# Kernel optimization log

Measured on AMD Instinct MI355X. Metric: run time of the kernel, lower is better.

The kernel has to match this reference:

```python
import jax, jax.numpy as jnp
import numpy as np
from jax.scipy.special import erfinv

N, F0, F1 = 256, 128, 64          # nodes, scalar channels, vector channels
RB, KSEQ, EMB = 32, 16, 32        # radial bins, seq window, pos-embed dim
RC = 24.0                         # radial_cut
NI = F0 + F1                      # num output irreps (per-irrep scalar gate)
CIN = F0 + F1 + 1 + F0            # 321 = per-l fan-in of the message Linear

# real l=2 CG matrices, e3nn component order: (xz, xy, y^2-(x^2+z^2)/2, yz, z^2-x^2)
_M = np.zeros((5, 3, 3), np.float32)
_M[0, 0, 2] = _M[0, 2, 0] = 1.0 / np.sqrt(10.0)
_M[1, 0, 1] = _M[1, 1, 0] = 1.0 / np.sqrt(10.0)
_M[2] = np.diag([-1.0, 2.0, -1.0]) / np.sqrt(30.0)
_M[3, 1, 2] = _M[3, 2, 1] = 1.0 / np.sqrt(10.0)
_M[4] = np.diag([-1.0, 0.0, 1.0]) / np.sqrt(10.0)
M2 = jnp.asarray(_M)

# e3nn-style normalized activation: silu / sqrt(E[silu(z)^2]), z ~ N(0,1)
_zs = jnp.sqrt(2.0) * erfinv(jnp.linspace(-1.0 + 1e-6, 1.0 - 1e-6, 100001))
C_SILU = jnp.sqrt(jnp.mean(jax.nn.silu(_zs) ** 2))

def nsilu(x):
    return jax.nn.silu(x) / C_SILU

def setup_inputs() -> dict:
    key = jax.random.key(0)
    ks = jax.random.split(key, 12)
    return {
        "feat": jax.random.normal(ks[0], (N, F0 + 3 * F1), jnp.float32),
        "coord": 8.0 * jax.random.normal(ks[1], (N, 3), jnp.float32),
        "W_msg0": jax.random.normal(ks[2], (CIN, F0), jnp.float32),
        "W_msg1": jax.random.normal(ks[3], (CIN, F1), jnp.float32),
        "embed_tbl": jax.random.normal(ks[4], (2 * KSEQ + 1, EMB), jnp.float32) / jnp.sqrt(2.0 * KSEQ + 1.0),
        "W_mlp1": jax.random.normal(ks[5], (EMB + RB + F0 + F0, RB), jnp.float32),
        "W_mlp2": jax.random.normal(ks[6], (RB, NI), jnp.float32),
        "W_out0": jax.random.normal(ks[7], (F0, F0), jnp.float32),
        "W_out1": jax.random.normal(ks[8], (F1, F1), jnp.float32),
        "W_move": jax.random.normal(ks[9], (F1, 1), jnp.float32),
        "mask": jax.random.randint(ks[10], (N,), 0, 2).astype(bool),
    }

def reference(feat, coord, W_msg0, W_msg1, embed_tbl, W_mlp1, W_mlp2, W_out0, W_out1, W_move, mask):
    n = feat.shape[0]
    s_in = feat[:, :F0]                       # [N,128] scalar irreps
    v_in = feat[:, F0:].reshape(n, F1, 3)     # [N,64,3] vector irreps
    cm = mask[:, None] & mask[None, :]
    cmf = cm.astype(feat.dtype)
    vec = (coord[:, None, :] - coord[None, :, :]) * cmf[..., None]   # [N,N,3]
    nsq = jnp.sum(vec ** 2, -1)
    dist = jnp.sqrt(jnp.where(nsq == 0.0, 1.0, nsq))
    x, y, z = vec[..., 0], vec[..., 1], vec[..., 2]
    # spherical harmonics, normalize=False, component normalization
    sh1 = jnp.sqrt(3.0) * vec
    sh2 = jnp.stack([jnp.sqrt(15.0) * x * z, jnp.sqrt(15.0) * x * y,
                     jnp.sqrt(5.0) * (y * y - 0.5 * (x * x + z * z)),
                     jnp.sqrt(15.0) * y * z, jnp.sqrt(15.0) / 2.0 * (z * z - x * x)], -1)
    # ---- message Linear over concat([TP(ang, feat_j), ang, feat_j]) ----
    # 0e inputs: [N,N,321]
    in0 = jnp.concatenate([
        cmf[..., None] * s_in[None, :, :],                        # 0e(sh) x 0e
        jnp.einsum('abd,bcd->abc', sh1, v_in) / jnp.sqrt(3.0),    # 1o x 1o -> 0e
        cmf[..., None],                                           # ang 0e (masked)
        jnp.broadcast_to(s_in[None], (n, n, F0)),                 # feat_j 0e
    ], -1)
    msg0 = jnp.einsum('abi,io->abo', in0, W_msg0) / jnp.sqrt(float(CIN))   # [N,N,128]
    # 1o inputs: [N,N,321,3]
    in1 = jnp.concatenate([
        cmf[..., None, None] * v_in[None],                                 # 0e x 1o
        sh1[:, :, None, :] * s_in[None, :, :, None],                       # 1o x 0e
        jnp.sqrt(3.0) * jnp.einsum('abm,mdk,bcd->abck', sh2, M2, v_in),    # 2e x 1o -> 1o
        sh1[:, :, None, :],                                                # ang 1o
        jnp.broadcast_to(v_in[None], (n, n, F1, 3)),                       # feat_j 1o
    ], 2)
    msg1 = jnp.einsum('abid,io->abod', in1, W_msg1) / jnp.sqrt(float(CIN))  # [N,N,64,3]
    # ---- radial / sequence gate ----
    values = jnp.linspace(0.0, RC, RB + 2)[1:-1]
    step = values[1] - values[0]
    rad = jnp.exp(-(((dist[..., None] - values) / step) ** 2)) / 1.12 * cmf[..., None]
    pos = jnp.arange(n)
    rel = pos[:, None] - pos[None, :]
    rel = jnp.where(jnp.abs(rel) <= KSEQ, rel, 0)
    rel = jnp.where(cm, rel, 0) + KSEQ
    pemb = embed_tbl[rel]                                                  # [N,N,32]
    gate_in = jnp.concatenate([pemb, rad,
                               jnp.broadcast_to(s_in[:, None, :], (n, n, F0)),
                               msg0], -1)                                  # [N,N,320]
    h = nsilu(jnp.einsum('abi,io->abo', gate_in, W_mlp1) / jnp.sqrt(float(gate_in.shape[-1])))
    gate = jnp.einsum('abi,io->abo', h, W_mlp2) / jnp.sqrt(float(RB))      # [N,N,192]
    msg0 = msg0 * gate[..., :F0] * cmf[..., None]
    msg1 = msg1 * gate[..., F0:, None] * cmf[..., None, None]
    # ---- masked mean aggregation over j ----
    cnt = jnp.sum(cmf, 1, keepdims=True)
    aggr0 = jnp.sum(msg0, 1) / (cnt + 1e-6)
    aggr1 = jnp.sum(msg1, 1) / (cnt[..., None] + 1e-6)
    keep = (cnt > 1).astype(feat.dtype)
    aggr0 = aggr0 * keep
    aggr1 = aggr1 * keep[..., None]
    # output Linear per irrep type
    f0 = aggr0 @ W_out0 / jnp.sqrt(float(F0))
    f1 = jnp.einsum('ncd,co->nod', aggr1, W_out1) / jnp.sqrt(float(F1))
    # coordinate update (move=True)
    coord_new = coord + 0.001 * jnp.einsum('ncd,co->nod', f1, W_move)[:, 0, :] / jnp.sqrt(float(F1))
    # residual + equivariant layer norm
    r0 = s_in + f0
    r1 = v_in + f1
    mu = jnp.mean(r0, -1, keepdims=True)
    n0 = (r0 - mu) / jnp.sqrt(jnp.var(r0, -1, keepdims=True) + 1e-6)
    rms = jnp.sqrt(jnp.mean(r1 ** 2, (-2, -1), keepdims=True) + 1e-6)
    n1 = r1 / rms
    return jnp.concatenate([n0, n1.reshape(n, -1), coord_new], -1)   # [N, 323]
```

## Files before the change

### kernel.cpp

```cpp
#include <hip/hip_runtime.h>
#include <math.h>

#define NN 256
#define NSPLIT 2

#define OFF_T0    0
#define OFF_TW    131072
#define OFF_T1A   163840
#define OFF_T1B   229376
#define OFF_S     294912
#define OFF_E     303104
#define OFF_CSP   305152
#define OFF_PART  305472
#define OFF_NA    469312
#define OFF_MASKD 469376

__device__ __forceinline__ float my_erfinv(float x){
    float w = -logf((1.0f - x) * (1.0f + x));
    float p;
    if (w < 5.0f) {
        w = w - 2.5f;
        p = 2.81022636e-08f;
        p = 3.43273939e-07f + p*w;
        p = -3.5233877e-06f + p*w;
        p = -4.39150654e-06f + p*w;
        p = 0.00021858087f  + p*w;
        p = -0.00125372503f + p*w;
        p = -0.00417768164f + p*w;
        p = 0.246640727f    + p*w;
        p = 1.50140941f     + p*w;
    } else {
        w = sqrtf(w) - 3.0f;
        p = -0.000200214257f;
        p = 0.000100950558f + p*w;
        p = 0.00134934322f  + p*w;
        p = -0.00367342844f + p*w;
        p = 0.00573950773f  + p*w;
        p = -0.0076224613f  + p*w;
        p = 0.00943887047f  + p*w;
        p = 1.00167406f     + p*w;
        p = 2.83297682f     + p*w;
    }
    return p * x;
}

__global__ __launch_bounds__(256) void precompute_kernel(
    const float* __restrict__ feat, const float* __restrict__ W0,
    const float* __restrict__ W1, const float* __restrict__ tbl,
    const float* __restrict__ Wm1, float* __restrict__ ws)
{
    int b = blockIdx.x, t = threadIdx.x;
    __shared__ float s_l[128], v_l[192];
    __shared__ float P0B_l[128], V0_l[3][128];
    __shared__ float red[256];

    if (b >= NN){
        int bi = b - NN;
        int lo = bi * 391;
        int hi = lo + 391; if (hi > 100001) hi = 100001;
        float acc = 0.f;
        for (int i = lo + t; i < hi; i += 256){
            float u = -0.999999f + (float)i * (1.999998f / 100000.0f);
            float z = 1.41421356237f * my_erfinv(u);
            float s = z / (1.0f + __expf(-z));
            acc += s * s;
        }
        red[t] = acc;
        __syncthreads();
        for (int off = 128; off >= 1; off >>= 1){
            if (t < off) red[t] += red[t + off];
            __syncthreads();
        }
        if (t == 0) ws[OFF_CSP + bi] = red[0];
        return;
    }

    for (int idx = t; idx < 320; idx += 256){
        float val = feat[b*320 + idx];
        if (idx < 128) s_l[idx] = val; else v_l[idx-128] = val;
    }
    __syncthreads();
    if (t < 128){
        int o = t;
        float p0 = W0[192*128 + o];
        #pragma unroll 4
        for (int i = 0; i < 128; i++){
            float s = s_l[i];
            p0 += s * (W0[i*128 + o] + W0[(193+i)*128 + o]);
        }
        float v0d[3];
        for (int d = 0; d < 3; d++){
            float v0 = 0.f;
            #pragma unroll 4
            for (int c = 0; c < 64; c++) v0 += v_l[c*3+d] * W0[(128+c)*128 + o];
            v0d[d] = v0;
        }
        P0B_l[o] = p0;
        V0_l[0][o] = v0d[0]; V0_l[1][o] = v0d[1]; V0_l[2][o] = v0d[2];
        ((float4*)(ws + OFF_T0))[b*128 + o] = make_float4(p0, v0d[0], v0d[1], v0d[2]);
    } else if (t < 192){
        int o = t - 128;
        float ac[3];
        for (int k = 0; k < 3; k++){
            float s = 0.f;
            #pragma unroll 4
            for (int c = 0; c < 64; c++){
                float v = v_l[c*3+k];
                s += v * (W1[c*64 + o] + W1[(257+c)*64 + o]);
            }
            ac[k] = s;
        }
        float p1 = W1[256*64 + o];
        #pragma unroll 4
        for (int c = 0; c < 128; c++) p1 += s_l[c] * W1[(64+c)*64 + o];
        float u1[3];
        for (int d = 0; d < 3; d++){
            float s = 0.f;
            #pragma unroll 4
            for (int c = 0; c < 64; c++) s += v_l[c*3+d] * W1[(192+c)*64 + o];
            u1[d] = 1.73205081f * s;
        }
        ((float4*)(ws + OFF_T1A))[b*64 + o] = make_float4(ac[0], ac[1], ac[2], p1);
        ((float4*)(ws + OFF_T1B))[b*64 + o] = make_float4(u1[0], u1[1], u1[2], 0.f);
    } else if (t < 224){
        int r = t - 192;
        float s = 0.f;
        #pragma unroll 4
        for (int i = 0; i < 128; i++) s += s_l[i] * Wm1[(64+i)*32 + r];
        ws[OFF_S + b*32 + r] = s;
        if (b < 33){
            float e = 0.f;
            #pragma unroll 4
            for (int k = 0; k < 32; k++) e += tbl[b*32 + k] * Wm1[k*32 + r];
            ws[OFF_E + b*32 + r] = e;
        }
    }
    __syncthreads();
    if (t < 32){
        int r = t;
        float pw = 0.f, vw0 = 0.f, vw1 = 0.f, vw2 = 0.f;
        #pragma unroll 4
        for (int o = 0; o < 128; o++){
            float w = Wm1[(192+o)*32 + r];
            pw  += P0B_l[o]  * w;
            vw0 += V0_l[0][o]* w;
            vw1 += V0_l[1][o]* w;
            vw2 += V0_l[2][o]* w;
        }
        ((float4*)(ws + OFF_TW))[b*32 + r] = make_float4(pw, vw0, vw1, vw2);
    }
}

__global__ __launch_bounds__(512) void main_kernel(
    const float* __restrict__ coord, const int* __restrict__ maskraw,
    const float* __restrict__ Wm1, const float* __restrict__ Wm2,
    float* __restrict__ ws, float* __restrict__ part)
{
    const int bid = blockIdx.x;
    const int a = bid >> 1;
    const int q = bid & 1;
    const int t = threadIdx.x;
    const int g = t >> 5;
    const int l = t & 31;

    __shared__ __align__(16) float smem_big[192*36];
    __shared__ __align__(16) float WT1[32*36];
    __shared__ __align__(16) float E_l[33*32];
    __shared__ __align__(16) float hsh[16*32];
    __shared__ __align__(16) float radsh[16*32];
    __shared__ int   blist[NN];
    __shared__ float cxl[NN], cyl[NN], czl[NN];
    __shared__ int   wcnt[4], wbase[4];
    __shared__ float cs_part[4];
    __shared__ int   na_sh, bflag_sh, maska_sh;
    __shared__ float invc_sh;

    for (int idx = t; idx < 6144; idx += 512){
        int r = idx / 192, o = idx - r*192;
        smem_big[o*36 + r] = Wm2[idx];
    }
    for (int idx = t; idx < 1024; idx += 512){
        int j = idx >> 5, l2 = idx & 31;
        WT1[l2*36 + j] = Wm1[1024 + idx];
    }
    for (int idx = t; idx < 1056; idx += 512) E_l[idx] = ws[OFF_E + idx];

    if (t == 0) bflag_sh = 0;
    __syncthreads();
    if (t < 64 && (maskraw[t] & 0xFFFFFFFE)) bflag_sh = 1;
    float cs_acc = (t < NN) ? ws[OFF_CSP + t] : 0.f;
    __syncthreads();
    const bool bytemode = bflag_sh != 0;

    int m_t = 0, pfx = 0;
    if (t < NN){
        if (bytemode){
            unsigned int w = (unsigned int)maskraw[t >> 2];
            m_t = ((w >> ((t & 3) * 8)) & 0xFFu) != 0;
        } else {
            m_t = maskraw[t] != 0;
        }
        if (t == a) maska_sh = m_t;
        if (bid == 0) ((int*)ws)[OFF_MASKD + t] = m_t;
        unsigned long long bal = __ballot(m_t != 0);
        int lane = t & 63;
        pfx = __popcll(bal & ((1ull << lane) - 1ull));
        if (lane == 0) wcnt[t >> 6] = __popcll(bal);
        #pragma unroll
        for (int off = 32; off >= 1; off >>= 1) cs_acc += __shfl_xor(cs_acc, off);
        if (lane == 0) cs_part[t >> 6] = cs_acc;
    }
    __syncthreads();
    if (t == 0){
        int s = 0;
        for (int w = 0; w < 4; w++){ wbase[w] = s; s += wcnt[w]; }
        na_sh = s;
        if (bid == 0) ((int*)ws)[OFF_NA] = s;
        float cstot = cs_part[0] + cs_part[1] + cs_part[2] + cs_part[3];
        invc_sh = 1.0f / sqrtf(cstot / 100001.0f);
    }
    __syncthreads();
    if (t < NN && m_t) blist[wbase[t >> 6] + pfx] = t;
    __syncthreads();
    const int na_all = na_sh;
    for (int idx = t; idx < na_all; idx += 512){
        int bb = blist[idx];
        cxl[idx] = coord[bb*3+0];
        cyl[idx] = coord[bb*3+1];
        czl[idx] = coord[bb*3+2];
    }
    __syncthreads();

    const float inv_c = invc_sh;
    const bool mask_a = maska_sh != 0;
    const float ca0 = coord[a*3+0], ca1 = coord[a*3+1], ca2 = coord[a*3+2];
    const float sar = ws[OFF_S + a*32 + l];

    const float ISC   = 0.055814557f;
    const float IS320 = 0.055901699f;

    float acc0[4] = {0.f,0.f,0.f,0.f};
    float acc1[2][3] = {{0.f,0.f,0.f},{0.f,0.f,0.f}};

    const int na_eff = mask_a ? na_all : 0;
    const int nq = (na_eff + NSPLIT - 1) / NSPLIT;
    const int base = q * nq;
    int cntq = na_eff - base;
    if (cntq < 0) cntq = 0;
    if (cntq > nq) cntq = nq;
    const int iters = (cntq + 15) >> 4;

    const float4* T0  = (const float4*)(ws + OFF_T0);
    const float4* TW  = (const float4*)(ws + OFF_TW);
    const float4* T1A = (const float4*)(ws + OFF_T1A);
    const float4* T1B = (const float4*)(ws + OFF_T1B);
    const float4* Wm2T4 = (const float4*)smem_big;
    const float4* WT14  = (const float4*)WT1;

    for (int i = 0; i < iters; i++){
        int il = i*16 + g;
        bool active = il < cntq;
        int idx = base + (active ? il : 0);
        int b = blist[idx];
        float cmf = active ? 1.0f : 0.0f;

        float vx = ca0 - cxl[idx], vy = ca1 - cyl[idx], vz = ca2 - czl[idx];
        float nsq = vx*vx + vy*vy + vz*vz;
        float dist = sqrtf(nsq == 0.0f ? 1.0f : nsq);
        float sh1x = 1.73205081f*vx, sh1y = 1.73205081f*vy, sh1z = 1.73205081f*vz;
        float s20 = 3.87298335f*vx*vz;
        float s21 = 3.87298335f*vx*vy;
        float s22 = 2.23606798f*(vy*vy - 0.5f*(vx*vx + vz*vz));
        float s23 = 3.87298335f*vy*vz;
        float s24 = 1.93649167f*(vz*vz - vx*vx);
        float Txx = -s22*0.182574186f - s24*0.316227766f;
        float Tyy =  s22*0.365148372f;
        float Tzz = -s22*0.182574186f + s24*0.316227766f;
        float Txy =  s21*0.316227766f;
        float Txz =  s20*0.316227766f;
        float Tyz =  s23*0.316227766f;

        float m0v[4];
        #pragma unroll
        for (int j = 0; j < 4; j++){
            float4 t0 = T0[b*128 + l + 32*j];
            m0v[j] = t0.x + vx*t0.y + vy*t0.z + vz*t0.w;
        }

        float vcen = 0.727272727f * (float)(l + 1);
        float ddr = (dist - vcen) * 1.375f;
        float rl = __expf(-ddr*ddr) * 0.892857143f * cmf;
        radsh[g*32 + l] = rl;
        float radw = 0.f;
        {
            const float4* rv = (const float4*)radsh + g*8;
            const float4* wv = WT14 + l*9;
            #pragma unroll
            for (int j4 = 0; j4 < 8; j4++){
                float4 r4 = rv[j4];
                float4 w4 = wv[j4];
                radw += r4.x*w4.x + r4.y*w4.y + r4.z*w4.z + r4.w*w4.w;
            }
        }

        int ir = a - b;
        if (ir > 16 || ir < -16) ir = 0;
        if (!active) ir = 0;
        ir += 16;
        float4 tw = TW[b*32 + l];
        float msgblk = tw.x + vx*tw.y + vy*tw.z + vz*tw.w;
        float pre = (E_l[ir*32 + l] + sar + radw + msgblk*ISC) * IS320;
        float h = pre / (1.0f + __expf(-pre)) * inv_c;
        hsh[g*32 + l] = h;

        float gg[6] = {0,0,0,0,0,0};
        {
            const float4* hv = (const float4*)hsh + g*8;
            #pragma unroll
            for (int r4 = 0; r4 < 8; r4++){
                float4 h4 = hv[r4];
                #pragma unroll
                for (int k = 0; k < 6; k++){
                    float4 w4 = Wm2T4[(l + 32*k)*9 + r4];
                    gg[k] += h4.x*w4.x + h4.y*w4.y + h4.z*w4.z + h4.w*w4.w;
                }
            }
        }
        #pragma unroll
        for (int k = 0; k < 6; k++) gg[k] *= cmf;

        #pragma unroll
        for (int j = 0; j < 4; j++) acc0[j] += m0v[j] * gg[j];

        #pragma unroll
        for (int jj = 0; jj < 2; jj++){
            float4 a1 = T1A[b*64 + l + 32*jj];
            float4 u1 = T1B[b*64 + l + 32*jj];
            float gv = gg[4+jj];
            float m10 = a1.x + sh1x*a1.w + Txx*u1.x + Txy*u1.y + Txz*u1.z;
            float m11 = a1.y + sh1y*a1.w + Txy*u1.x + Tyy*u1.y + Tyz*u1.z;
            float m12 = a1.z + sh1z*a1.w + Txz*u1.x + Tyz*u1.y + Tzz*u1.z;
            acc1[jj][0] += m10 * gv;
            acc1[jj][1] += m11 * gv;
            acc1[jj][2] += m12 * gv;
        }
    }

    #pragma unroll
    for (int j = 0; j < 4; j++) acc0[j] += __shfl_xor(acc0[j], 32);
    #pragma unroll
    for (int jj = 0; jj < 2; jj++)
        #pragma unroll
        for (int k = 0; k < 3; k++) acc1[jj][k] += __shfl_xor(acc1[jj][k], 32);

    __syncthreads();
    float* red0 = smem_big;
    float* red1 = smem_big + 1024;
    const int wv = t >> 6;
    if ((t & 63) < 32){
        #pragma unroll
        for (int j = 0; j < 4; j++) red0[wv*128 + l + 32*j] = acc0[j];
        #pragma unroll
        for (int jj = 0; jj < 2; jj++)
            #pragma unroll
            for (int k = 0; k < 3; k++) red1[wv*192 + (l + 32*jj)*3 + k] = acc1[jj][k];
    }
    __syncthreads();

    if (t < 320){
        float s = 0.f;
        if (t < 128){
            #pragma unroll
            for (int w = 0; w < 8; w++) s += red0[w*128 + t];
        } else {
            #pragma unroll
            for (int w = 0; w < 8; w++) s += red1[w*192 + t - 128];
        }
        part[bid*320 + t] = s;
    }
}

__global__ __launch_bounds__(256) void epilogue_kernel(
    const float* __restrict__ feat, const float* __restrict__ coord,
    const float* __restrict__ Wout0, const float* __restrict__ Wout1,
    const float* __restrict__ Wmove,
    const float* __restrict__ ws, const float* __restrict__ part,
    float* __restrict__ out)
{
    const int a = blockIdx.x;
    const int t = threadIdx.x;

    __shared__ float aggr[320];
    __shared__ float r0_l[128];
    __shared__ float r1_l[192];
    __shared__ float f1_l[192];
    __shared__ float stats[8];

    const int cnt_i = ((const int*)ws)[OFF_NA];
    const int ma    = ((const int*)ws)[OFF_MASKD + a];
    const float cntv = ma ? (float)cnt_i : 0.0f;
    const float inv = (cntv > 1.0f) ? 1.0f / (cntv + 1e-6f) : 0.0f;
    const float SCALE = 0.055814557f * 0.176776695f;

    for (int idx = t; idx < 320; idx += 256){
        float s = 0.f;
        #pragma unroll
        for (int qq = 0; qq < NSPLIT; qq++) s += part[(a*NSPLIT+qq)*320 + idx];
        aggr[idx] = s * SCALE * inv;
    }
    __syncthreads();

    if (t < 128){
        float f = 0.f;
        #pragma unroll 4
        for (int c = 0; c < 128; c++) f += aggr[c] * Wout0[c*128 + t];
        r0_l[t] = feat[a*320 + t] + f * 0.088388348f;
    } else if (t < 192){
        int o = t - 128;
        float fv0 = 0.f, fv1 = 0.f, fv2 = 0.f;
        #pragma unroll 4
        for (int c = 0; c < 64; c++){
            float w = Wout1[c*64 + o];
            fv0 += aggr[128 + c*3+0] * w;
            fv1 += aggr[128 + c*3+1] * w;
            fv2 += aggr[128 + c*3+2] * w;
        }
        fv0 *= 0.125f; fv1 *= 0.125f; fv2 *= 0.125f;
        f1_l[o*3+0] = fv0; f1_l[o*3+1] = fv1; f1_l[o*3+2] = fv2;
        r1_l[o*3+0] = feat[a*320 + 128 + o*3+0] + fv0;
        r1_l[o*3+1] = feat[a*320 + 128 + o*3+1] + fv1;
        r1_l[o*3+2] = feat[a*320 + 128 + o*3+2] + fv2;
    }
    __syncthreads();

    if (t < 64){
        float x0 = r0_l[t], x1 = r0_l[t+64];
        float s0 = x0 + x1, sq = x0*x0 + x1*x1;
        float y0 = r1_l[t*3], y1 = r1_l[t*3+1], y2 = r1_l[t*3+2];
        float s1 = y0*y0 + y1*y1 + y2*y2;
        float wm = Wmove[t];
        float d0 = f1_l[t*3+0]*wm, d1 = f1_l[t*3+1]*wm, d2 = f1_l[t*3+2]*wm;
        #pragma unroll
        for (int off = 32; off >= 1; off >>= 1){
            s0 += __shfl_xor(s0, off);
            sq += __shfl_xor(sq, off);
            s1 += __shfl_xor(s1, off);
            d0 += __shfl_xor(d0, off);
            d1 += __shfl_xor(d1, off);
            d2 += __shfl_xor(d2, off);
        }
        if (t == 0){
            float mu = s0 * (1.0f/128.0f);
            float var = sq * (1.0f/128.0f) - mu*mu;
            stats[0] = mu;
            stats[1] = 1.0f / sqrtf(var + 1e-6f);
            stats[2] = 1.0f / sqrtf(s1 * (1.0f/192.0f) + 1e-6f);
            stats[3] = d0; stats[4] = d1; stats[5] = d2;
        }
    }
    __syncthreads();

    float* orow = out + a*323;
    for (int idx = t; idx < 323; idx += 256){
        float v;
        if (idx < 128)      v = (r0_l[idx] - stats[0]) * stats[1];
        else if (idx < 320) v = r1_l[idx-128] * stats[2];
        else                v = coord[a*3 + (idx-320)] + 0.000125f * stats[3 + (idx-320)];
        orow[idx] = v;
    }
}

extern "C" void kernel_launch(void* const* d_in, const int* in_sizes, int n_in,
                              void* d_out, int out_size, void* d_ws, size_t ws_size,
                              hipStream_t stream)
{
    const float* feat  = (const float*)d_in[0];
    const float* coord = (const float*)d_in[1];
    const float* W0    = (const float*)d_in[2];
    const float* W1    = (const float*)d_in[3];
    const float* tbl   = (const float*)d_in[4];
    const float* Wm1   = (const float*)d_in[5];
    const float* Wm2   = (const float*)d_in[6];
    const float* Wout0 = (const float*)d_in[7];
    const float* Wout1 = (const float*)d_in[8];
    const float* Wmove = (const float*)d_in[9];
    const int*   mask  = (const int*)d_in[10];
    float* ws  = (float*)d_ws;
    float* out = (float*)d_out;

    precompute_kernel<<<NN + 256, 256, 0, stream>>>(feat, W0, W1, tbl, Wm1, ws);
    main_kernel<<<NN*NSPLIT, 512, 0, stream>>>(coord, mask, Wm1, Wm2, ws, ws + OFF_PART);
    epilogue_kernel<<<NN, 256, 0, stream>>>(feat, coord, Wout0, Wout1, Wmove,
                                            ws, ws + OFF_PART, out);
}
```

Measured before the change: 203.1 us.

## Fuse three kernels into one cooperative kernel and redistribute pair work over active nodes

Merges the precompute, main and epilogue kernels into a single cooperative kernel separated by grid-wide syncs, with a three-launch fallback if the cooperative launch fails. The pair phase now assigns the 512 blocks only to masked-in nodes, each split into GRID/na chunks, rather than a fixed 2-way split over all nodes that leaves masked-out nodes idle. Blocks shrink from 512 to 256 threads with 8 pairs per iteration, and shared memory is reused across phases through a union-like buffer. The aim is to remove launch gaps and the wasted work on masked nodes, at the cost of grid-sync overhead and an occupancy limit of two blocks per CU.

Result: slower. 259.4 us (+27.7%).

```diff
diff --git a/kernel.cpp b/kernel.cpp
--- a/kernel.cpp
+++ b/kernel.cpp
@@ -1,8 +1,13 @@
 #include <hip/hip_runtime.h>
+#include <hip/hip_cooperative_groups.h>
 #include <math.h>
 
+namespace cg = cooperative_groups;
+
 #define NN 256
-#define NSPLIT 2
+#define GRID 512
+#define BLK 256
+#define SMEM_BYTES 43008
 
 #define OFF_T0    0
 #define OFF_TW    131072
@@ -12,8 +17,6 @@
 #define OFF_E     303104
 #define OFF_CSP   305152
 #define OFF_PART  305472
-#define OFF_NA    469312
-#define OFF_MASKD 469376
 
 __device__ __forceinline__ float my_erfinv(float x){
     float w = -logf((1.0f - x) * (1.0f + x));
@@ -44,195 +47,213 @@
     return p * x;
 }
 
-__global__ __launch_bounds__(256) void precompute_kernel(
+struct SA {
+    float s_l[128];
+    float v_l[192];
+    float P0B[128];
+    float V0[3][128];
+};
+struct SCs {
+    float red[BLK];
+};
+struct SB {
+    float wm2t[192*36];
+    float wt1[32*36];
+    float el[1056];
+    float hsh[BLK];
+    float radsh[BLK];
+    float cx[256], cy[256], cz[256];
+    int   blist[256];
+    int   wcnt[4], wbase[4];
+    float cs_part[4];
+    int   na, bflag;
+    float invc;
+};
+struct SD {
+    float aggr[320];
+    float r0[128];
+    float r1[192];
+    float f1[192];
+    float stats[8];
+    int   wcnt[4], wbase[4];
+    int   na, aidx, ma, bflag;
+};
+
+__device__ __forceinline__ void phaseA(
+    int bid, int t, char* smem,
     const float* __restrict__ feat, const float* __restrict__ W0,
-    const float* __restrict__ W1, const float* __restrict__ tbl,
-    const float* __restrict__ Wm1, float* __restrict__ ws)
-{
-    int b = blockIdx.x, t = threadIdx.x;
-    __shared__ float s_l[128], v_l[192];
-    __shared__ float P0B_l[128], V0_l[3][128];
-    __shared__ float red[256];
-
-    if (b >= NN){
-        int bi = b - NN;
-        int lo = bi * 391;
+    const float* __restrict__ W1,   const float* __restrict__ tbl,
+    const float* __restrict__ Wm1,  float* __restrict__ ws)
+{
+    if (bid < NN){
+        SA& A = *reinterpret_cast<SA*>(smem);
+        const int b = bid;
+        for (int idx = t; idx < 320; idx += BLK){
+            float val = feat[b*320 + idx];
+            if (idx < 128) A.s_l[idx] = val; else A.v_l[idx-128] = val;
+        }
+        __syncthreads();
+        if (t < 128){
+            int o = t;
+            float p0 = W0[192*128 + o];
+            #pragma unroll 4
+            for (int i = 0; i < 128; i++){
+                float s = A.s_l[i];
+                p0 += s * (W0[i*128 + o] + W0[(193+i)*128 + o]);
+            }
+            float v0d[3];
+            for (int d = 0; d < 3; d++){
+                float v0 = 0.f;
+                #pragma unroll 4
+                for (int c = 0; c < 64; c++) v0 += A.v_l[c*3+d] * W0[(128+c)*128 + o];
+                v0d[d] = v0;
+            }
+            A.P0B[o] = p0;
+            A.V0[0][o] = v0d[0]; A.V0[1][o] = v0d[1]; A.V0[2][o] = v0d[2];
+            ((float4*)(ws + OFF_T0))[b*128 + o] = make_float4(p0, v0d[0], v0d[1], v0d[2]);
+        } else if (t < 192){
+            int o = t - 128;
+            float ac[3];
+            for (int k = 0; k < 3; k++){
+                float s = 0.f;
+                #pragma unroll 4
+                for (int c = 0; c < 64; c++){
+                    float v = A.v_l[c*3+k];
+                    s += v * (W1[c*64 + o] + W1[(257+c)*64 + o]);
+                }
+                ac[k] = s;
+            }
+            float p1 = W1[256*64 + o];
+            #pragma unroll 4
+            for (int c = 0; c < 128; c++) p1 += A.s_l[c] * W1[(64+c)*64 + o];
+            float u1[3];
+            for (int d = 0; d < 3; d++){
+                float s = 0.f;
+                #pragma unroll 4
+                for (int c = 0; c < 64; c++) s += A.v_l[c*3+d] * W1[(192+c)*64 + o];
+                u1[d] = 1.73205081f * s;
+            }
+            ((float4*)(ws + OFF_T1A))[b*64 + o] = make_float4(ac[0], ac[1], ac[2], p1);
+            ((float4*)(ws + OFF_T1B))[b*64 + o] = make_float4(u1[0], u1[1], u1[2], 0.f);
+        } else if (t < 224){
+            int r = t - 192;
+            float s = 0.f;
+            #pragma unroll 4
+            for (int i = 0; i < 128; i++) s += A.s_l[i] * Wm1[(64+i)*32 + r];
+            ws[OFF_S + b*32 + r] = s;
+            if (b < 33){
+                float e = 0.f;
+                #pragma unroll 4
+                for (int k = 0; k < 32; k++) e += tbl[b*32 + k] * Wm1[k*32 + r];
+                ws[OFF_E + b*32 + r] = e;
+            }
+        }
+        __syncthreads();
+        if (t < 32){
+            int r = t;
+            float pw = 0.f, vw0 = 0.f, vw1 = 0.f, vw2 = 0.f;
+            #pragma unroll 4
+            for (int o = 0; o < 128; o++){
+                float w = Wm1[(192+o)*32 + r];
+                pw  += A.P0B[o]  * w;
+                vw0 += A.V0[0][o]* w;
+                vw1 += A.V0[1][o]* w;
+                vw2 += A.V0[2][o]* w;
+            }
+            ((float4*)(ws + OFF_TW))[b*32 + r] = make_float4(pw, vw0, vw1, vw2);
+        }
+    } else {
+        SCs& C = *reinterpret_cast<SCs*>(smem);
+        int slice = bid - NN;
+        int lo = slice * 391;
         int hi = lo + 391; if (hi > 100001) hi = 100001;
         float acc = 0.f;
-        for (int i = lo + t; i < hi; i += 256){
+        for (int i = lo + t; i < hi; i += BLK){
             float u = -0.999999f + (float)i * (1.999998f / 100000.0f);
             float z = 1.41421356237f * my_erfinv(u);
             float s = z / (1.0f + __expf(-z));
             acc += s * s;
         }
-        red[t] = acc;
+        C.red[t] = acc;
         __syncthreads();
-        for (int off = 128; off >= 1; off >>= 1){
-            if (t < off) red[t] += red[t + off];
+        for (int off = BLK/2; off >= 1; off >>= 1){
+            if (t < off) C.red[t] += C.red[t + off];
             __syncthreads();
         }
-        if (t == 0) ws[OFF_CSP + bi] = red[0];
-        return;
-    }
-
-    for (int idx = t; idx < 320; idx += 256){
-        float val = feat[b*320 + idx];
-        if (idx < 128) s_l[idx] = val; else v_l[idx-128] = val;
-    }
-    __syncthreads();
-    if (t < 128){
-        int o = t;
-        float p0 = W0[192*128 + o];
-        #pragma unroll 4
-        for (int i = 0; i < 128; i++){
-            float s = s_l[i];
-            p0 += s * (W0[i*128 + o] + W0[(193+i)*128 + o]);
-        }
-        float v0d[3];
-        for (int d = 0; d < 3; d++){
-            float v0 = 0.f;
-            #pragma unroll 4
-            for (int c = 0; c < 64; c++) v0 += v_l[c*3+d] * W0[(128+c)*128 + o];
-            v0d[d] = v0;
-        }
-        P0B_l[o] = p0;
-        V0_l[0][o] = v0d[0]; V0_l[1][o] = v0d[1]; V0_l[2][o] = v0d[2];
-        ((float4*)(ws + OFF_T0))[b*128 + o] = make_float4(p0, v0d[0], v0d[1], v0d[2]);
-    } else if (t < 192){
-        int o = t - 128;
-        float ac[3];
-        for (int k = 0; k < 3; k++){
-            float s = 0.f;
-            #pragma unroll 4
-            for (int c = 0; c < 64; c++){
-                float v = v_l[c*3+k];
-                s += v * (W1[c*64 + o] + W1[(257+c)*64 + o]);
-            }
-            ac[k] = s;
-        }
-        float p1 = W1[256*64 + o];
-        #pragma unroll 4
-        for (int c = 0; c < 128; c++) p1 += s_l[c] * W1[(64+c)*64 + o];
-        float u1[3];
-        for (int d = 0; d < 3; d++){
-            float s = 0.f;
-            #pragma unroll 4
-            for (int c = 0; c < 64; c++) s += v_l[c*3+d] * W1[(192+c)*64 + o];
-            u1[d] = 1.73205081f * s;
-        }
-        ((float4*)(ws + OFF_T1A))[b*64 + o] = make_float4(ac[0], ac[1], ac[2], p1);
-        ((float4*)(ws + OFF_T1B))[b*64 + o] = make_float4(u1[0], u1[1], u1[2], 0.f);
-    } else if (t < 224){
-        int r = t - 192;
-        float s = 0.f;
-        #pragma unroll 4
-        for (int i = 0; i < 128; i++) s += s_l[i] * Wm1[(64+i)*32 + r];
-        ws[OFF_S + b*32 + r] = s;
-        if (b < 33){
-            float e = 0.f;
-            #pragma unroll 4
-            for (int k = 0; k < 32; k++) e += tbl[b*32 + k] * Wm1[k*32 + r];
-            ws[OFF_E + b*32 + r] = e;
-        }
-    }
-    __syncthreads();
-    if (t < 32){
-        int r = t;
-        float pw = 0.f, vw0 = 0.f, vw1 = 0.f, vw2 = 0.f;
-        #pragma unroll 4
-        for (int o = 0; o < 128; o++){
-            float w = Wm1[(192+o)*32 + r];
-            pw  += P0B_l[o]  * w;
-            vw0 += V0_l[0][o]* w;
-            vw1 += V0_l[1][o]* w;
-            vw2 += V0_l[2][o]* w;
-        }
-        ((float4*)(ws + OFF_TW))[b*32 + r] = make_float4(pw, vw0, vw1, vw2);
-    }
-}
-
-__global__ __launch_bounds__(512) void main_kernel(
+        if (t == 0) ws[OFF_CSP + slice] = C.red[0];
+    }
+}
+
+__device__ __forceinline__ void phaseB(
+    int bid, int t, char* smem,
     const float* __restrict__ coord, const int* __restrict__ maskraw,
-    const float* __restrict__ Wm1, const float* __restrict__ Wm2,
-    float* __restrict__ ws, float* __restrict__ part)
-{
-    const int bid = blockIdx.x;
-    const int a = bid >> 1;
-    const int q = bid & 1;
-    const int t = threadIdx.x;
+    const float* __restrict__ Wm1,   const float* __restrict__ Wm2,
+    float* __restrict__ ws)
+{
+    SB& B = *reinterpret_cast<SB*>(smem);
     const int g = t >> 5;
     const int l = t & 31;
 
-    __shared__ __align__(16) float smem_big[192*36];
-    __shared__ __align__(16) float WT1[32*36];
-    __shared__ __align__(16) float E_l[33*32];
-    __shared__ __align__(16) float hsh[16*32];
-    __shared__ __align__(16) float radsh[16*32];
-    __shared__ int   blist[NN];
-    __shared__ float cxl[NN], cyl[NN], czl[NN];
-    __shared__ int   wcnt[4], wbase[4];
-    __shared__ float cs_part[4];
-    __shared__ int   na_sh, bflag_sh, maska_sh;
-    __shared__ float invc_sh;
-
-    for (int idx = t; idx < 6144; idx += 512){
+    for (int idx = t; idx < 6144; idx += BLK){
         int r = idx / 192, o = idx - r*192;
-        smem_big[o*36 + r] = Wm2[idx];
-    }
-    for (int idx = t; idx < 1024; idx += 512){
+        B.wm2t[o*36 + r] = Wm2[idx];
+    }
+    for (int idx = t; idx < 1024; idx += BLK){
         int j = idx >> 5, l2 = idx & 31;
-        WT1[l2*36 + j] = Wm1[1024 + idx];
-    }
-    for (int idx = t; idx < 1056; idx += 512) E_l[idx] = ws[OFF_E + idx];
-
-    if (t == 0) bflag_sh = 0;
-    __syncthreads();
-    if (t < 64 && (maskraw[t] & 0xFFFFFFFE)) bflag_sh = 1;
-    float cs_acc = (t < NN) ? ws[OFF_CSP + t] : 0.f;
-    __syncthreads();
-    const bool bytemode = bflag_sh != 0;
+        B.wt1[l2*36 + j] = Wm1[1024 + idx];
+    }
+    for (int idx = t; idx < 1056; idx += BLK) B.el[idx] = ws[OFF_E + idx];
+
+    if (t == 0) B.bflag = 0;
+    __syncthreads();
+    if (t < 64 && (maskraw[t] & 0xFFFFFFFE)) B.bflag = 1;
+    float cs_acc = ws[OFF_CSP + t];
+    __syncthreads();
+    const bool bytemode = B.bflag != 0;
 
     int m_t = 0, pfx = 0;
-    if (t < NN){
+    {
         if (bytemode){
             unsigned int w = (unsigned int)maskraw[t >> 2];
             m_t = ((w >> ((t & 3) * 8)) & 0xFFu) != 0;
         } else {
             m_t = maskraw[t] != 0;
         }
-        if (t == a) maska_sh = m_t;
-        if (bid == 0) ((int*)ws)[OFF_MASKD + t] = m_t;
         unsigned long long bal = __ballot(m_t != 0);
         int lane = t & 63;
         pfx = __popcll(bal & ((1ull << lane) - 1ull));
-        if (lane == 0) wcnt[t >> 6] = __popcll(bal);
+        if (lane == 0) B.wcnt[t >> 6] = __popcll(bal);
         #pragma unroll
         for (int off = 32; off >= 1; off >>= 1) cs_acc += __shfl_xor(cs_acc, off);
-        if (lane == 0) cs_part[t >> 6] = cs_acc;
+        if (lane == 0) B.cs_part[t >> 6] = cs_acc;
     }
     __syncthreads();
     if (t == 0){
         int s = 0;
-        for (int w = 0; w < 4; w++){ wbase[w] = s; s += wcnt[w]; }
-        na_sh = s;
-        if (bid == 0) ((int*)ws)[OFF_NA] = s;
-        float cstot = cs_part[0] + cs_part[1] + cs_part[2] + cs_part[3];
-        invc_sh = 1.0f / sqrtf(cstot / 100001.0f);
-    }
-    __syncthreads();
-    if (t < NN && m_t) blist[wbase[t >> 6] + pfx] = t;
-    __syncthreads();
-    const int na_all = na_sh;
-    for (int idx = t; idx < na_all; idx += 512){
-        int bb = blist[idx];
-        cxl[idx] = coord[bb*3+0];
-        cyl[idx] = coord[bb*3+1];
-        czl[idx] = coord[bb*3+2];
-    }
-    __syncthreads();
-
-    const float inv_c = invc_sh;
-    const bool mask_a = maska_sh != 0;
+        for (int w = 0; w < 4; w++){ B.wbase[w] = s; s += B.wcnt[w]; }
+        B.na = s;
+        float cstot = B.cs_part[0] + B.cs_part[1] + B.cs_part[2] + B.cs_part[3];
+        B.invc = 1.0f / sqrtf(cstot / 100001.0f);
+    }
+    __syncthreads();
+    if (m_t) B.blist[B.wbase[t >> 6] + pfx] = t;
+    __syncthreads();
+    const int na = B.na;
+    for (int idx = t; idx < na; idx += BLK){
+        int bb = B.blist[idx];
+        B.cx[idx] = coord[bb*3+0];
+        B.cy[idx] = coord[bb*3+1];
+        B.cz[idx] = coord[bb*3+2];
+    }
+    __syncthreads();
+
+    const int ns = (na > 0) ? max(1, GRID / na) : 1;
+    const int ai = bid / ns;
+    const int chunk = bid - ai * ns;
+    const bool active_blk = ai < na;
+    const int a = B.blist[active_blk ? ai : 0];
+
+    const float inv_c = B.invc;
     const float ca0 = coord[a*3+0], ca1 = coord[a*3+1], ca2 = coord[a*3+2];
     const float sar = ws[OFF_S + a*32 + l];
 
@@ -242,29 +263,28 @@
     float acc0[4] = {0.f,0.f,0.f,0.f};
     float acc1[2][3] = {{0.f,0.f,0.f},{0.f,0.f,0.f}};
 
-    const int na_eff = mask_a ? na_all : 0;
-    const int nq = (na_eff + NSPLIT - 1) / NSPLIT;
-    const int base = q * nq;
-    int cntq = na_eff - base;
+    const int nq = (na + ns - 1) / ns;
+    const int base = chunk * nq;
+    int cntq = active_blk ? (na - base) : 0;
     if (cntq < 0) cntq = 0;
     if (cntq > nq) cntq = nq;
-    const int iters = (cntq + 15) >> 4;
+    const int iters = (cntq + 7) >> 3;
 
     const float4* T0  = (const float4*)(ws + OFF_T0);
     const float4* TW  = (const float4*)(ws + OFF_TW);
     const float4* T1A = (const float4*)(ws + OFF_T1A);
     const float4* T1B = (const float4*)(ws + OFF_T1B);
-    const float4* Wm2T4 = (const float4*)smem_big;
-    const float4* WT14  = (const float4*)WT1;
+    const float4* Wm2T4 = (const float4*)B.wm2t;
+    const float4* WT14  = (const float4*)B.wt1;
 
     for (int i = 0; i < iters; i++){
-        int il = i*16 + g;
+        int il = i*8 + g;
         bool active = il < cntq;
         int idx = base + (active ? il : 0);
-        int b = blist[idx];
+        int b = B.blist[idx];
         float cmf = active ? 1.0f : 0.0f;
 
-        float vx = ca0 - cxl[idx], vy = ca1 - cyl[idx], vz = ca2 - czl[idx];
+        float vx = ca0 - B.cx[idx], vy = ca1 - B.cy[idx], vz = ca2 - B.cz[idx];
         float nsq = vx*vx + vy*vy + vz*vz;
         float dist = sqrtf(nsq == 0.0f ? 1.0f : nsq);
         float sh1x = 1.73205081f*vx, sh1y = 1.73205081f*vy, sh1z = 1.73205081f*vz;
@@ -290,10 +310,10 @@
         float vcen = 0.727272727f * (float)(l + 1);
         float ddr = (dist - vcen) * 1.375f;
         float rl = __expf(-ddr*ddr) * 0.892857143f * cmf;
-        radsh[g*32 + l] = rl;
+        B.radsh[g*32 + l] = rl;
         float radw = 0.f;
         {
-            const float4* rv = (const float4*)radsh + g*8;
+            const float4* rv = (const float4*)B.radsh + g*8;
             const float4* wv = WT14 + l*9;
             #pragma unroll
             for (int j4 = 0; j4 < 8; j4++){
@@ -309,13 +329,13 @@
         ir += 16;
         float4 tw = TW[b*32 + l];
         float msgblk = tw.x + vx*tw.y + vy*tw.z + vz*tw.w;
-        float pre = (E_l[ir*32 + l] + sar + radw + msgblk*ISC) * IS320;
+        float pre = (B.el[ir*32 + l] + sar + radw + msgblk*ISC) * IS320;
         float h = pre / (1.0f + __expf(-pre)) * inv_c;
-        hsh[g*32 + l] = h;
+        B.hsh[g*32 + l] = h;
 
         float gg[6] = {0,0,0,0,0,0};
         {
-            const float4* hv = (const float4*)hsh + g*8;
+            const float4* hv = (const float4*)B.hsh + g*8;
             #pragma unroll
             for (int r4 = 0; r4 < 8; r4++){
                 float4 h4 = hv[r4];
@@ -354,8 +374,8 @@
         for (int k = 0; k < 3; k++) acc1[jj][k] += __shfl_xor(acc1[jj][k], 32);
 
     __syncthreads();
-    float* red0 = smem_big;
-    float* red1 = smem_big + 1024;
+    float* red0 = B.wm2t;
+    float* red1 = B.wm2t + 512;
     const int wv = t >> 6;
     if ((t & 63) < 32){
         #pragma unroll
@@ -367,79 +387,110 @@
     }
     __syncthreads();
 
-    if (t < 320){
+    for (int idx = t; idx < 320; idx += BLK){
         float s = 0.f;
-        if (t < 128){
+        if (idx < 128){
             #pragma unroll
-            for (int w = 0; w < 8; w++) s += red0[w*128 + t];
+            for (int w = 0; w < 4; w++) s += red0[w*128 + idx];
         } else {
             #pragma unroll
-            for (int w = 0; w < 8; w++) s += red1[w*192 + t - 128];
-        }
-        part[bid*320 + t] = s;
-    }
-}
-
-__global__ __launch_bounds__(256) void epilogue_kernel(
-    const float* __restrict__ feat, const float* __restrict__ coord,
+            for (int w = 0; w < 4; w++) s += red1[w*192 + idx - 128];
+        }
+        ws[OFF_PART + bid*320 + idx] = s;
+    }
+}
+
+__device__ __forceinline__ void phaseC(
+    int bid, int t, char* smem,
+    const float* __restrict__ feat,  const float* __restrict__ coord,
+    const int* __restrict__ maskraw,
     const float* __restrict__ Wout0, const float* __restrict__ Wout1,
-    const float* __restrict__ Wmove,
-    const float* __restrict__ ws, const float* __restrict__ part,
+    const float* __restrict__ Wmove, const float* __restrict__ ws,
     float* __restrict__ out)
 {
-    const int a = blockIdx.x;
-    const int t = threadIdx.x;
-
-    __shared__ float aggr[320];
-    __shared__ float r0_l[128];
-    __shared__ float r1_l[192];
-    __shared__ float f1_l[192];
-    __shared__ float stats[8];
-
-    const int cnt_i = ((const int*)ws)[OFF_NA];
-    const int ma    = ((const int*)ws)[OFF_MASKD + a];
-    const float cntv = ma ? (float)cnt_i : 0.0f;
+    if (bid >= NN) return;
+    SD& D = *reinterpret_cast<SD*>(smem);
+    const int a = bid;
+
+    if (t == 0) D.bflag = 0;
+    __syncthreads();
+    if (t < 64 && (maskraw[t] & 0xFFFFFFFE)) D.bflag = 1;
+    __syncthreads();
+    const bool bytemode = D.bflag != 0;
+    int m_t = 0, pfx = 0;
+    {
+        if (bytemode){
+            unsigned int w = (unsigned int)maskraw[t >> 2];
+            m_t = ((w >> ((t & 3) * 8)) & 0xFFu) != 0;
+        } else {
+            m_t = maskraw[t] != 0;
+        }
+        unsigned long long bal = __ballot(m_t != 0);
+        int lane = t & 63;
+        pfx = __popcll(bal & ((1ull << lane) - 1ull));
+        if (lane == 0) D.wcnt[t >> 6] = __popcll(bal);
+    }
+    __syncthreads();
+    if (t == 0){
+        int s = 0;
+        for (int w = 0; w < 4; w++){ D.wbase[w] = s; s += D.wcnt[w]; }
+        D.na = s;
+    }
+    __syncthreads();
+    if (t == a){
+        D.ma = m_t;
+        D.aidx = D.wbase[t >> 6] + pfx;
+    }
+    __syncthreads();
+
+    const int na = D.na;
+    const int ma = D.ma;
+    const int ns = (na > 0) ? max(1, GRID / na) : 1;
+    const int aidx = D.aidx;
+    const float cntv = ma ? (float)na : 0.0f;
     const float inv = (cntv > 1.0f) ? 1.0f / (cntv + 1e-6f) : 0.0f;
     const float SCALE = 0.055814557f * 0.176776695f;
 
-    for (int idx = t; idx < 320; idx += 256){
+    for (int idx = t; idx < 320; idx += BLK){
         float s = 0.f;
-        #pragma unroll
-        for (int qq = 0; qq < NSPLIT; qq++) s += part[(a*NSPLIT+qq)*320 + idx];
-        aggr[idx] = s * SCALE * inv;
+        if (ma){
+            for (int j = 0; j < ns; j++)
+                s += ws[OFF_PART + (aidx*ns + j)*320 + idx];
+        }
+        D.aggr[idx] = s * SCALE * inv;
     }
     __syncthreads();
 
     if (t < 128){
         float f = 0.f;
         #pragma unroll 4
-        for (int c = 0; c < 128; c++) f += aggr[c] * Wout0[c*128 + t];
-        r0_l[t] = feat[a*320 + t] + f * 0.088388348f;
+        for (int c = 0; c < 128; c++) f += D.aggr[c] * Wout0[c*128 + t];
+        D.r0[t] = feat[a*320 + t] + f * 0.088388348f;
     } else if (t < 192){
         int o = t - 128;
         float fv0 = 0.f, fv1 = 0.f, fv2 = 0.f;
         #pragma unroll 4
         for (int c = 0; c < 64; c++){
             float w = Wout1[c*64 + o];
-            fv0 += aggr[128 + c*3+0] * w;
-            fv1 += aggr[128 + c*3+1] * w;
-            fv2 += aggr[128 + c*3+2] * w;
+            fv0 += D.aggr[128 + c*3+0] * w;
+            fv1 += D.aggr[128 + c*3+1] * w;
+            fv2 += D.aggr[128 + c*3+2] * w;
         }
         fv0 *= 0.125f; fv1 *= 0.125f; fv2 *= 0.125f;
-        f1_l[o*3+0] = fv0; f1_l[o*3+1] = fv1; f1_l[o*3+2] = fv2;
-        r1_l[o*3+0] = feat[a*320 + 128 + o*3+0] + fv0;
-        r1_l[o*3+1] = feat[a*320 + 128 + o*3+1] + fv1;
-        r1_l[o*3+2] = feat[a*320 + 128 + o*3+2] + fv2;
+        D.f1[o*3+0] = fv0; D.f1[o*3+1] = fv1; D.f1[o*3+2] = fv2;
+        D.r1[o*3+0] = feat[a*320 + 128 + o*3+0] + fv0;
+        D.r1[o*3+1] = feat[a*320 + 128 + o*3+1] + fv1;
+        D.r1[o*3+2] = feat[a*320 + 128 + o*3+2] + fv2;
     }
     __syncthreads();
 
     if (t < 64){
-        float x0 = r0_l[t], x1 = r0_l[t+64];
+        float x0 = D.r0[t], x1 = D.r0[t+64];
         float s0 = x0 + x1, sq = x0*x0 + x1*x1;
-        float y0 = r1_l[t*3], y1 = r1_l[t*3+1], y2 = r1_l[t*3+2];
+        float y0 = D.r1[t*3], y1 = D.r1[t*3+1], y2 = D.r1[t*3+2];
         float s1 = y0*y0 + y1*y1 + y2*y2;
         float wm = Wmove[t];
-        float d0 = f1_l[t*3+0]*wm, d1 = f1_l[t*3+1]*wm, d2 = f1_l[t*3+2]*wm;
+        float d0 = D.f1[t*3+0]*wm, d1 = D.f1[t*3+1]*wm, d2 = D.f1[t*3+2]*wm;
         #pragma unroll
         for (int off = 32; off >= 1; off >>= 1){
             s0 += __shfl_xor(s0, off);
@@ -452,22 +503,76 @@
         if (t == 0){
             float mu = s0 * (1.0f/128.0f);
             float var = sq * (1.0f/128.0f) - mu*mu;
-            stats[0] = mu;
-            stats[1] = 1.0f / sqrtf(var + 1e-6f);
-            stats[2] = 1.0f / sqrtf(s1 * (1.0f/192.0f) + 1e-6f);
-            stats[3] = d0; stats[4] = d1; stats[5] = d2;
+            D.stats[0] = mu;
+            D.stats[1] = 1.0f / sqrtf(var + 1e-6f);
+            D.stats[2] = 1.0f / sqrtf(s1 * (1.0f/192.0f) + 1e-6f);
+            D.stats[3] = d0; D.stats[4] = d1; D.stats[5] = d2;
         }
     }
     __syncthreads();
 
     float* orow = out + a*323;
-    for (int idx = t; idx < 323; idx += 256){
+    for (int idx = t; idx < 323; idx += BLK){
         float v;
-        if (idx < 128)      v = (r0_l[idx] - stats[0]) * stats[1];
-        else if (idx < 320) v = r1_l[idx-128] * stats[2];
-        else                v = coord[a*3 + (idx-320)] + 0.000125f * stats[3 + (idx-320)];
+        if (idx < 128)      v = (D.r0[idx] - D.stats[0]) * D.stats[1];
+        else if (idx < 320) v = D.r1[idx-128] * D.stats[2];
+        else                v = coord[a*3 + (idx-320)] + 0.000125f * D.stats[3 + (idx-320)];
         orow[idx] = v;
     }
+}
+
+__global__ void __launch_bounds__(BLK, 2) fused_kernel(
+    const float* __restrict__ feat, const float* __restrict__ coord,
+    const float* __restrict__ W0,   const float* __restrict__ W1,
+    const float* __restrict__ tbl,  const float* __restrict__ Wm1,
+    const float* __restrict__ Wm2,  const float* __restrict__ Wout0,
+    const float* __restrict__ Wout1,const float* __restrict__ Wmove,
+    const int* __restrict__ maskraw, float* __restrict__ ws,
+    float* __restrict__ out)
+{
+    __shared__ __align__(16) char smem[SMEM_BYTES];
+    static_assert(sizeof(SA)  <= SMEM_BYTES, "SA");
+    static_assert(sizeof(SCs) <= SMEM_BYTES, "SCs");
+    static_assert(sizeof(SB)  <= SMEM_BYTES, "SB");
+    static_assert(sizeof(SD)  <= SMEM_BYTES, "SD");
+    cg::grid_group grid = cg::this_grid();
+    const int bid = blockIdx.x, t = threadIdx.x;
+
+    phaseA(bid, t, smem, feat, W0, W1, tbl, Wm1, ws);
+    grid.sync();
+    phaseB(bid, t, smem, coord, maskraw, Wm1, Wm2, ws);
+    grid.sync();
+    phaseC(bid, t, smem, feat, coord, maskraw, Wout0, Wout1, Wmove, ws, out);
+}
+
+__global__ void __launch_bounds__(BLK, 2) kernelA(
+    const float* __restrict__ feat, const float* __restrict__ W0,
+    const float* __restrict__ W1,   const float* __restrict__ tbl,
+    const float* __restrict__ Wm1,  float* __restrict__ ws)
+{
+    __shared__ __align__(16) char smem[SMEM_BYTES];
+    phaseA(blockIdx.x, threadIdx.x, smem, feat, W0, W1, tbl, Wm1, ws);
+}
+
+__global__ void __launch_bounds__(BLK, 2) kernelB(
+    const float* __restrict__ coord, const int* __restrict__ maskraw,
+    const float* __restrict__ Wm1,   const float* __restrict__ Wm2,
+    float* __restrict__ ws)
+{
+    __shared__ __align__(16) char smem[SMEM_BYTES];
+    phaseB(blockIdx.x, threadIdx.x, smem, coord, maskraw, Wm1, Wm2, ws);
+}
+
+__global__ void __launch_bounds__(BLK, 2) kernelC(
+    const float* __restrict__ feat,  const float* __restrict__ coord,
+    const int* __restrict__ maskraw,
+    const float* __restrict__ Wout0, const float* __restrict__ Wout1,
+    const float* __restrict__ Wmove, const float* __restrict__ ws,
+    float* __restrict__ out)
+{
+    __shared__ __align__(16) char smem[SMEM_BYTES];
+    phaseC(blockIdx.x, threadIdx.x, smem, feat, coord, maskraw,
+           Wout0, Wout1, Wmove, ws, out);
 }
 
 extern "C" void kernel_launch(void* const* d_in, const int* in_sizes, int n_in,
@@ -488,8 +593,18 @@
     float* ws  = (float*)d_ws;
     float* out = (float*)d_out;
 
-    precompute_kernel<<<NN + 256, 256, 0, stream>>>(feat, W0, W1, tbl, Wm1, ws);
-    main_kernel<<<NN*NSPLIT, 512, 0, stream>>>(coord, mask, Wm1, Wm2, ws, ws + OFF_PART);
-    epilogue_kernel<<<NN, 256, 0, stream>>>(feat, coord, Wout0, Wout1, Wmove,
-                                            ws, ws + OFF_PART, out);
-}
+    void* args[] = {
+        (void*)&feat, (void*)&coord, (void*)&W0, (void*)&W1, (void*)&tbl,
+        (void*)&Wm1, (void*)&Wm2, (void*)&Wout0, (void*)&Wout1, (void*)&Wmove,
+        (void*)&mask, (void*)&ws, (void*)&out
+    };
+    hipError_t err = hipLaunchCooperativeKernel((const void*)fused_kernel,
+                                                dim3(GRID), dim3(BLK),
+                                                args, 0, stream);
+    if (err != hipSuccess){
+        kernelA<<<GRID, BLK, 0, stream>>>(feat, W0, W1, tbl, Wm1, ws);
+        kernelB<<<GRID, BLK, 0, stream>>>(coord, mask, Wm1, Wm2, ws);
+        kernelC<<<NN,   BLK, 0, stream>>>(feat, coord, mask, Wout0, Wout1,
+                                          Wmove, ws, out);
+    }
+}
```

## Fuse epilogue into main kernel and drop the per-node j-split

Applied to the files above, without the earlier changes.

Merges the epilogue (output linears, residual, layer norm, coordinate update) into the main per-node kernel and removes the NSPLIT=2 split over neighbours, so each block handles one node end to end. This removes one kernel launch and the partial-sum round trip through global workspace. In exchange the grid halves to 256 blocks of 512 threads, which cuts parallelism on a GPU with many CUs, and each block runs twice as many neighbour iterations serially.

Measured after the change: 181.2 us. 1.12x faster.

```diff
diff --git a/kernel.cpp b/kernel.cpp
--- a/kernel.cpp
+++ b/kernel.cpp
@@ -2,7 +2,6 @@
 #include <math.h>
 
 #define NN 256
-#define NSPLIT 2
 
 #define OFF_T0    0
 #define OFF_TW    131072
@@ -11,9 +10,6 @@
 #define OFF_S     294912
 #define OFF_E     303104
 #define OFF_CSP   305152
-#define OFF_PART  305472
-#define OFF_NA    469312
-#define OFF_MASKD 469376
 
 __device__ __forceinline__ float my_erfinv(float x){
     float w = -logf((1.0f - x) * (1.0f + x));
@@ -151,25 +147,26 @@
     }
 }
 
-__global__ __launch_bounds__(512) void main_kernel(
-    const float* __restrict__ coord, const int* __restrict__ maskraw,
-    const float* __restrict__ Wm1, const float* __restrict__ Wm2,
-    float* __restrict__ ws, float* __restrict__ part)
+__global__ __launch_bounds__(512) void mainepi_kernel(
+    const float* __restrict__ feat,  const float* __restrict__ coord,
+    const int* __restrict__ maskraw,
+    const float* __restrict__ Wm1,   const float* __restrict__ Wm2,
+    const float* __restrict__ Wout0, const float* __restrict__ Wout1,
+    const float* __restrict__ Wmove,
+    const float* __restrict__ ws,    float* __restrict__ out)
 {
-    const int bid = blockIdx.x;
-    const int a = bid >> 1;
-    const int q = bid & 1;
+    const int a = blockIdx.x;
     const int t = threadIdx.x;
     const int g = t >> 5;
     const int l = t & 31;
 
-    __shared__ __align__(16) float smem_big[192*36];
+    __shared__ __align__(16) float big[192*36];
     __shared__ __align__(16) float WT1[32*36];
     __shared__ __align__(16) float E_l[33*32];
-    __shared__ __align__(16) float hsh[16*32];
-    __shared__ __align__(16) float radsh[16*32];
+    __shared__ __align__(16) float hsh[512];
+    __shared__ __align__(16) float radsh[512];
+    __shared__ float cxl[NN], cyl[NN], czl[NN];
     __shared__ int   blist[NN];
-    __shared__ float cxl[NN], cyl[NN], czl[NN];
     __shared__ int   wcnt[4], wbase[4];
     __shared__ float cs_part[4];
     __shared__ int   na_sh, bflag_sh, maska_sh;
@@ -177,7 +174,7 @@
 
     for (int idx = t; idx < 6144; idx += 512){
         int r = idx / 192, o = idx - r*192;
-        smem_big[o*36 + r] = Wm2[idx];
+        big[o*36 + r] = Wm2[idx];
     }
     for (int idx = t; idx < 1024; idx += 512){
         int j = idx >> 5, l2 = idx & 31;
@@ -201,7 +198,6 @@
             m_t = maskraw[t] != 0;
         }
         if (t == a) maska_sh = m_t;
-        if (bid == 0) ((int*)ws)[OFF_MASKD + t] = m_t;
         unsigned long long bal = __ballot(m_t != 0);
         int lane = t & 63;
         pfx = __popcll(bal & ((1ull << lane) - 1ull));
@@ -215,15 +211,14 @@
         int s = 0;
         for (int w = 0; w < 4; w++){ wbase[w] = s; s += wcnt[w]; }
         na_sh = s;
-        if (bid == 0) ((int*)ws)[OFF_NA] = s;
         float cstot = cs_part[0] + cs_part[1] + cs_part[2] + cs_part[3];
         invc_sh = 1.0f / sqrtf(cstot / 100001.0f);
     }
     __syncthreads();
     if (t < NN && m_t) blist[wbase[t >> 6] + pfx] = t;
     __syncthreads();
-    const int na_all = na_sh;
-    for (int idx = t; idx < na_all; idx += 512){
+    const int na = na_sh;
+    for (int idx = t; idx < na; idx += 512){
         int bb = blist[idx];
         cxl[idx] = coord[bb*3+0];
         cyl[idx] = coord[bb*3+1];
@@ -242,25 +237,20 @@
     float acc0[4] = {0.f,0.f,0.f,0.f};
     float acc1[2][3] = {{0.f,0.f,0.f},{0.f,0.f,0.f}};
 
-    const int na_eff = mask_a ? na_all : 0;
-    const int nq = (na_eff + NSPLIT - 1) / NSPLIT;
-    const int base = q * nq;
-    int cntq = na_eff - base;
-    if (cntq < 0) cntq = 0;
-    if (cntq > nq) cntq = nq;
-    const int iters = (cntq + 15) >> 4;
+    const int cnt = mask_a ? na : 0;
+    const int iters = (cnt + 15) >> 4;
 
     const float4* T0  = (const float4*)(ws + OFF_T0);
     const float4* TW  = (const float4*)(ws + OFF_TW);
     const float4* T1A = (const float4*)(ws + OFF_T1A);
     const float4* T1B = (const float4*)(ws + OFF_T1B);
-    const float4* Wm2T4 = (const float4*)smem_big;
+    const float4* Wm2T4 = (const float4*)big;
     const float4* WT14  = (const float4*)WT1;
 
     for (int i = 0; i < iters; i++){
         int il = i*16 + g;
-        bool active = il < cntq;
-        int idx = base + (active ? il : 0);
+        bool active = il < cnt;
+        int idx = active ? il : 0;
         int b = blist[idx];
         float cmf = active ? 1.0f : 0.0f;
 
@@ -354,8 +344,14 @@
         for (int k = 0; k < 3; k++) acc1[jj][k] += __shfl_xor(acc1[jj][k], 32);
 
     __syncthreads();
-    float* red0 = smem_big;
-    float* red1 = smem_big + 1024;
+    float* red0  = big;
+    float* red1  = big + 1024;
+    float* aggr  = big + 2560;
+    float* r0_l  = big + 2880;
+    float* r1_l  = big + 3008;
+    float* f1_l  = big + 3200;
+    float* stats = big + 3392;
+
     const int wv = t >> 6;
     if ((t & 63) < 32){
         #pragma unroll
@@ -367,45 +363,19 @@
     }
     __syncthreads();
 
-    if (t < 320){
+    const float cntv = mask_a ? (float)na : 0.0f;
+    const float inv = (cntv > 1.0f) ? 1.0f / (cntv + 1e-6f) : 0.0f;
+    const float SCALE = 0.055814557f * 0.176776695f;
+
+    for (int idx = t; idx < 320; idx += 512){
         float s = 0.f;
-        if (t < 128){
+        if (idx < 128){
             #pragma unroll
-            for (int w = 0; w < 8; w++) s += red0[w*128 + t];
+            for (int w = 0; w < 8; w++) s += red0[w*128 + idx];
         } else {
             #pragma unroll
-            for (int w = 0; w < 8; w++) s += red1[w*192 + t - 128];
-        }
-        part[bid*320 + t] = s;
-    }
-}
-
-__global__ __launch_bounds__(256) void epilogue_kernel(
-    const float* __restrict__ feat, const float* __restrict__ coord,
-    const float* __restrict__ Wout0, const float* __restrict__ Wout1,
-    const float* __restrict__ Wmove,
-    const float* __restrict__ ws, const float* __restrict__ part,
-    float* __restrict__ out)
-{
-    const int a = blockIdx.x;
-    const int t = threadIdx.x;
-
-    __shared__ float aggr[320];
-    __shared__ float r0_l[128];
-    __shared__ float r1_l[192];
-    __shared__ float f1_l[192];
-    __shared__ float stats[8];
-
-    const int cnt_i = ((const int*)ws)[OFF_NA];
-    const int ma    = ((const int*)ws)[OFF_MASKD + a];
-    const float cntv = ma ? (float)cnt_i : 0.0f;
-    const float inv = (cntv > 1.0f) ? 1.0f / (cntv + 1e-6f) : 0.0f;
-    const float SCALE = 0.055814557f * 0.176776695f;
-
-    for (int idx = t; idx < 320; idx += 256){
-        float s = 0.f;
-        #pragma unroll
-        for (int qq = 0; qq < NSPLIT; qq++) s += part[(a*NSPLIT+qq)*320 + idx];
+            for (int w = 0; w < 8; w++) s += red1[w*192 + idx - 128];
+        }
         aggr[idx] = s * SCALE * inv;
     }
     __syncthreads();
@@ -461,7 +431,7 @@
     __syncthreads();
 
     float* orow = out + a*323;
-    for (int idx = t; idx < 323; idx += 256){
+    for (int idx = t; idx < 323; idx += 512){
         float v;
         if (idx < 128)      v = (r0_l[idx] - stats[0]) * stats[1];
         else if (idx < 320) v = r1_l[idx-128] * stats[2];
@@ -489,7 +459,6 @@
     float* out = (float*)d_out;
 
     precompute_kernel<<<NN + 256, 256, 0, stream>>>(feat, W0, W1, tbl, Wm1, ws);
-    main_kernel<<<NN*NSPLIT, 512, 0, stream>>>(coord, mask, Wm1, Wm2, ws, ws + OFF_PART);
-    epilogue_kernel<<<NN, 256, 0, stream>>>(feat, coord, Wout0, Wout1, Wmove,
-                                            ws, ws + OFF_PART, out);
+    mainepi_kernel<<<NN, 512, 0, stream>>>(feat, coord, mask, Wm1, Wm2,
+                                           Wout0, Wout1, Wmove, ws, out);
 }
```
